# Kernel optimization log

Measured on AMD Instinct MI355X. Metric: run time of the kernel, lower is better.

The kernel has to match this reference:

```python
import jax, jax.numpy as jnp
import numpy as np

N, M, K, C = 1000, 2000, 10, 80
IOU_THRESHOLD = 0.5
EPS = 1e-7


def setup_inputs() -> dict:
    key = jax.random.key(0)
    k1, k2, k3, k4, k5, k6, k7 = jax.random.split(key, 7)
    # pred boxes: realistic xyxy boxes in a 1000x1000 image
    cxy = jax.random.uniform(k1, (N, 2), minval=0.0, maxval=1000.0)
    wh = jax.random.uniform(k2, (N, 2), minval=20.0, maxval=100.0)
    pred_box = jnp.concatenate([cxy - wh / 2, cxy + wh / 2], axis=1)  # [N,4]
    pred = jnp.concatenate([pred_box, jax.random.uniform(k3, (N, 2))], axis=1)  # [N,6]
    # dropout passes: jittered copies of pred boxes (guarantees IoU>0.5 match)
    # followed by M-N random boxes
    copies = pred_box[None, :, :] + jax.random.normal(k4, (K, N, 4)) * 1.0  # [K,N,4]
    rc = jax.random.uniform(k5, (K, M - N, 2), minval=0.0, maxval=1000.0)
    rwh = jax.random.uniform(k6, (K, M - N, 2), minval=20.0, maxval=100.0)
    rand_box = jnp.concatenate([rc - rwh / 2, rc + rwh / 2], axis=2)  # [K,M-N,4]
    boxes = jnp.concatenate([copies, rand_box], axis=1)  # [K,M,4]
    dropout_preds = jnp.concatenate([boxes, jnp.ones((K, M, 2), jnp.float32)], axis=2)
    # per-box class probability rows (softmax-normalized, strictly positive)
    dropout_cls_confs = jax.nn.softmax(jax.random.normal(k7, (K, M, C)), axis=-1)
    return {
        "pred": pred.astype(jnp.float32),
        "dropout_preds": dropout_preds.astype(jnp.float32),
        "dropout_cls_confs": dropout_cls_confs.astype(jnp.float32),
    }


def _pairwise_iou(b1, b2):
    # b1: [N,4] xyxy, b2: [K,M,4] xyxy -> iou [K,N,M]
    ix1 = jnp.maximum(b1[None, :, None, 0], b2[:, None, :, 0])
    iy1 = jnp.maximum(b1[None, :, None, 1], b2[:, None, :, 1])
    ix2 = jnp.minimum(b1[None, :, None, 2], b2[:, None, :, 2])
    iy2 = jnp.minimum(b1[None, :, None, 3], b2[:, None, :, 3])
    inter = jnp.clip(ix2 - ix1, 0.0) * jnp.clip(iy2 - iy1, 0.0)  # [K,N,M]
    area1 = (b1[:, 2] - b1[:, 0]) * (b1[:, 3] - b1[:, 1])  # [N]
    area2 = (b2[..., 2] - b2[..., 0]) * (b2[..., 3] - b2[..., 1])  # [K,M]
    return inter / (area1[None, :, None] + area2[:, None, :] - inter + EPS)


def reference(pred, dropout_preds, dropout_cls_confs):
    n_classes = dropout_cls_confs.shape[-1]
    inv_n = 1.0 / n_classes
    max_entropy = -n_classes * (inv_n * jnp.log(jnp.float32(inv_n)))  # == log(C)

    iou = _pairwise_iou(pred[:, :4], dropout_preds[:, :, :4])  # [K,N,M]
    mask = iou > IOU_THRESHOLD  # [K,N,M]
    matched = jnp.any(mask, axis=-1)  # [K,N] any match in pass k for pred n
    first = jnp.argmax(mask, axis=-1)  # [K,N] index of FIRST match (break semantics)

    # gather the matched class-confidence row per (pass, pred): [K,N,C]
    rows = jnp.take_along_axis(dropout_cls_confs, first[:, :, None], axis=1)
    entropy = -jnp.sum(rows * jnp.log(rows), axis=-1)  # [K,N]
    u = 1.0 - entropy / max_entropy  # [K,N]

    matched_f = matched.astype(u.dtype)
    cnt = jnp.sum(matched_f, axis=0)  # [N]
    sum_u = jnp.sum(u * matched_f, axis=0)  # [N]
    # no-match fallback in original yields NaN (entropy of zeros row)
    semantic_uncertainty = jnp.where(cnt > 0, sum_u / jnp.maximum(cnt, 1.0), jnp.nan)
    return semantic_uncertainty
```

## Files before the change

kernel.cpp:

```cpp
#include <hip/hip_runtime.h>
#include <math.h>

#define N_PRED 1000
#define M_BOX  2000
#define K_PASS 10
#define C_CLS  80
#define IOU_THR 0.5f
#define EPS_IOU 1e-7f

#define P_PRED 4
#define BLK_T  (K_PASS * 64)
#define N_BLK  (N_PRED / P_PRED)

#define IDX_INF 0x7fffffff

__global__ __launch_bounds__(BLK_T)
void ue_cls_kernel(const float* __restrict__ pred,
                   const float* __restrict__ dpreds,
                   const float* __restrict__ dconfs,
                   float* __restrict__ out)
{
    const int k    = threadIdx.x >> 6;
    const int lane = threadIdx.x & 63;
    const int n0   = blockIdx.x * P_PRED;

    __shared__ float s_u[K_PASS][P_PRED];
    __shared__ float s_m[K_PASS][P_PRED];

    float px1[P_PRED], py1[P_PRED], px2[P_PRED], py2[P_PRED], a1[P_PRED];
    #pragma unroll
    for (int p = 0; p < P_PRED; ++p) {
        const float* pr = pred + (n0 + p) * 6;
        px1[p] = pr[0]; py1[p] = pr[1]; px2[p] = pr[2]; py2[p] = pr[3];
        a1[p] = (px2[p] - px1[p]) * (py2[p] - py1[p]);
    }

    const long kbase = (long)k * M_BOX;
    const float2* dp2 = (const float2*)dpreds;

    int firstI[P_PRED];
    #pragma unroll
    for (int p = 0; p < P_PRED; ++p) firstI[p] = IDX_INF;

    const int L = (((n0 + P_PRED - 1) >> 6) << 6) + 64;
    for (int c0 = 0; c0 < L; c0 += 64) {
        const int m = c0 + lane;
        const long i2 = (kbase + m) * 3;
        const float2 a = dp2[i2];
        const float2 b = dp2[i2 + 1];
        const float area2 = (b.x - a.x) * (b.y - a.y);
        #pragma unroll
        for (int p = 0; p < P_PRED; ++p) {
            const float ix1 = fmaxf(px1[p], a.x);
            const float iy1 = fmaxf(py1[p], a.y);
            const float ix2 = fminf(px2[p], b.x);
            const float iy2 = fminf(py2[p], b.y);
            const float inter = fmaxf(ix2 - ix1, 0.0f) * fmaxf(iy2 - iy1, 0.0f);
            const float den = a1[p] + area2 - inter + EPS_IOU;
            if (inter > 0.5f * den) firstI[p] = min(firstI[p], m);
        }
    }
    #pragma unroll
    for (int off = 32; off > 0; off >>= 1) {
        #pragma unroll
        for (int p = 0; p < P_PRED; ++p)
            firstI[p] = min(firstI[p], __shfl_xor(firstI[p], off, 64));
    }

    bool need = false;
    #pragma unroll
    for (int p = 0; p < P_PRED; ++p) need = need || (firstI[p] == IDX_INF);
    if (need) {
        for (int c0 = L; c0 < M_BOX; c0 += 64) {
            const int m = c0 + lane;
            const bool valid = (m < M_BOX);
            const long i2 = (kbase + (valid ? m : M_BOX - 1)) * 3;
            const float2 a = dp2[i2];
            const float2 b = dp2[i2 + 1];
            const float area2 = (b.x - a.x) * (b.y - a.y);
            #pragma unroll
            for (int p = 0; p < P_PRED; ++p) {
                const float ix1 = fmaxf(px1[p], a.x);
                const float iy1 = fmaxf(py1[p], a.y);
                const float ix2 = fminf(px2[p], b.x);
                const float iy2 = fminf(py2[p], b.y);
                const float inter = fmaxf(ix2 - ix1, 0.0f) * fmaxf(iy2 - iy1, 0.0f);
                const float den = a1[p] + area2 - inter + EPS_IOU;
                if (valid && inter > 0.5f * den) firstI[p] = min(firstI[p], m);
            }
        }
        #pragma unroll
        for (int off = 32; off > 0; off >>= 1) {
            #pragma unroll
            for (int p = 0; p < P_PRED; ++p)
                firstI[p] = min(firstI[p], __shfl_xor(firstI[p], off, 64));
        }
    }

    const float inv_n  = 1.0f / (float)C_CLS;
    const float max_en = -(float)C_CLS * (inv_n * logf(inv_n));
    float um[P_PRED], mt[P_PRED];
    #pragma unroll
    for (int p = 0; p < P_PRED; ++p) {
        um[p] = 0.0f; mt[p] = 0.0f;
        if (firstI[p] != IDX_INF) {
            mt[p] = 1.0f;
            const float* row = dconfs + (kbase + firstI[p]) * (long)C_CLS;
            float local = 0.0f;
            {
                const float v = row[lane];
                local -= v * logf(v);
            }
            if (lane < C_CLS - 64) {
                const float v = row[64 + lane];
                local -= v * logf(v);
            }
            #pragma unroll
            for (int off = 32; off > 0; off >>= 1)
                local += __shfl_xor(local, off, 64);
            um[p] = 1.0f - local / max_en;
        }
    }

    if (lane == 0) {
        #pragma unroll
        for (int p = 0; p < P_PRED; ++p) {
            s_u[k][p] = um[p] * mt[p];
            s_m[k][p] = mt[p];
        }
    }
    __syncthreads();

    if (threadIdx.x < P_PRED) {
        const int t = threadIdx.x;
        float cnt = 0.0f, su = 0.0f;
        #pragma unroll
        for (int kk = 0; kk < K_PASS; ++kk) { su += s_u[kk][t]; cnt += s_m[kk][t]; }
        out[n0 + t] = (cnt > 0.0f) ? (su / fmaxf(cnt, 1.0f)) : __builtin_nanf("");
    }
}

extern "C" void kernel_launch(void* const* d_in, const int* in_sizes, int n_in,
                              void* d_out, int out_size, void* d_ws, size_t ws_size,
                              hipStream_t stream) {
    const float* pred   = (const float*)d_in[0];
    const float* dpreds = (const float*)d_in[1];
    const float* dconfs = (const float*)d_in[2];
    float* out = (float*)d_out;

    ue_cls_kernel<<<dim3(N_BLK), dim3(BLK_T), 0, stream>>>(pred, dpreds, dconfs, out);
}
```

Baseline: 70.95 us.

## Process one prediction per block with ballot-based early-exit first-match search

The kernel now launches one block per prediction instead of one block per four predictions, which quadruples the block count and shortens each wave's serial dependency chain. The IoU scan unrolls two 64-column chunks per iteration. It uses a wave ballot with count-trailing-zeros to find the first match and break out immediately, replacing per-lane min tracking followed by a shuffle reduction. The trade-off is that pred-box loads and per-block overhead are repeated four times more often, and imbalance between waves that scan short and long column ranges remains.

```diff
diff --git a/kernel.cpp b/kernel.cpp
--- a/kernel.cpp
+++ b/kernel.cpp
@@ -5,13 +5,9 @@
 #define M_BOX  2000
 #define K_PASS 10
 #define C_CLS  80
-#define IOU_THR 0.5f
 #define EPS_IOU 1e-7f
 
-#define P_PRED 4
 #define BLK_T  (K_PASS * 64)
-#define N_BLK  (N_PRED / P_PRED)
-
 #define IDX_INF 0x7fffffff
 
 __global__ __launch_bounds__(BLK_T)
@@ -20,123 +16,115 @@
                    const float* __restrict__ dconfs,
                    float* __restrict__ out)
 {
+    const int n    = blockIdx.x;
     const int k    = threadIdx.x >> 6;
     const int lane = threadIdx.x & 63;
-    const int n0   = blockIdx.x * P_PRED;
 
-    __shared__ float s_u[K_PASS][P_PRED];
-    __shared__ float s_m[K_PASS][P_PRED];
+    __shared__ float s_u[K_PASS];
+    __shared__ float s_m[K_PASS];
 
-    float px1[P_PRED], py1[P_PRED], px2[P_PRED], py2[P_PRED], a1[P_PRED];
-    #pragma unroll
-    for (int p = 0; p < P_PRED; ++p) {
-        const float* pr = pred + (n0 + p) * 6;
-        px1[p] = pr[0]; py1[p] = pr[1]; px2[p] = pr[2]; py2[p] = pr[3];
-        a1[p] = (px2[p] - px1[p]) * (py2[p] - py1[p]);
+    const float* pr = pred + n * 6;
+    const float px1 = pr[0], py1 = pr[1], px2 = pr[2], py2 = pr[3];
+    const float a1  = (px2 - px1) * (py2 - py1);
+
+    const int kbase = k * M_BOX;
+    const float2* dp2 = (const float2*)dpreds;
+
+    const int L = ((n >> 6) + 1) << 6;
+    int first = IDX_INF;
+    int c0 = 0;
+    for (; c0 < L; c0 += 128) {
+        const int iA = (kbase + c0 + lane) * 3;
+        const int iB = iA + 64 * 3;
+        const float2 aA = dp2[iA];
+        const float2 bA = dp2[iA + 1];
+        const float2 aB = dp2[iB];
+        const float2 bB = dp2[iB + 1];
+
+        const float areaA = (bA.x - aA.x) * (bA.y - aA.y);
+        const float ix1A = fmaxf(px1, aA.x);
+        const float iy1A = fmaxf(py1, aA.y);
+        const float ix2A = fminf(px2, bA.x);
+        const float iy2A = fminf(py2, bA.y);
+        const float interA = fmaxf(ix2A - ix1A, 0.0f) * fmaxf(iy2A - iy1A, 0.0f);
+        const float denA = a1 + areaA - interA + EPS_IOU;
+
+        const float areaB = (bB.x - aB.x) * (bB.y - aB.y);
+        const float ix1B = fmaxf(px1, aB.x);
+        const float iy1B = fmaxf(py1, aB.y);
+        const float ix2B = fminf(px2, bB.x);
+        const float iy2B = fminf(py2, bB.y);
+        const float interB = fmaxf(ix2B - ix1B, 0.0f) * fmaxf(iy2B - iy1B, 0.0f);
+        const float denB = a1 + areaB - interB + EPS_IOU;
+
+        const unsigned long long hitA = __ballot(interA > 0.5f * denA);
+        const unsigned long long hitB = __ballot(interB > 0.5f * denB);
+        if (hitA) { first = c0 + __builtin_ctzll(hitA); break; }
+        if (hitB) { first = c0 + 64 + __builtin_ctzll(hitB); break; }
     }
 
-    const long kbase = (long)k * M_BOX;
-    const float2* dp2 = (const float2*)dpreds;
+    if (first == IDX_INF) {
+        for (; c0 < M_BOX; c0 += 128) {
+            const int mA = c0 + lane;
+            const int mB = mA + 64;
+            const bool vA = (mA < M_BOX);
+            const bool vB = (mB < M_BOX);
+            const int iA = (kbase + (vA ? mA : 0)) * 3;
+            const int iB = (kbase + (vB ? mB : 0)) * 3;
+            const float2 aA = dp2[iA];
+            const float2 bA = dp2[iA + 1];
+            const float2 aB = dp2[iB];
+            const float2 bB = dp2[iB + 1];
 
-    int firstI[P_PRED];
-    #pragma unroll
-    for (int p = 0; p < P_PRED; ++p) firstI[p] = IDX_INF;
+            const float areaA = (bA.x - aA.x) * (bA.y - aA.y);
+            const float interA = fmaxf(fminf(px2, bA.x) - fmaxf(px1, aA.x), 0.0f)
+                               * fmaxf(fminf(py2, bA.y) - fmaxf(py1, aA.y), 0.0f);
+            const float denA = a1 + areaA - interA + EPS_IOU;
 
-    const int L = (((n0 + P_PRED - 1) >> 6) << 6) + 64;
-    for (int c0 = 0; c0 < L; c0 += 64) {
-        const int m = c0 + lane;
-        const long i2 = (kbase + m) * 3;
-        const float2 a = dp2[i2];
-        const float2 b = dp2[i2 + 1];
-        const float area2 = (b.x - a.x) * (b.y - a.y);
-        #pragma unroll
-        for (int p = 0; p < P_PRED; ++p) {
-            const float ix1 = fmaxf(px1[p], a.x);
-            const float iy1 = fmaxf(py1[p], a.y);
-            const float ix2 = fminf(px2[p], b.x);
-            const float iy2 = fminf(py2[p], b.y);
-            const float inter = fmaxf(ix2 - ix1, 0.0f) * fmaxf(iy2 - iy1, 0.0f);
-            const float den = a1[p] + area2 - inter + EPS_IOU;
-            if (inter > 0.5f * den) firstI[p] = min(firstI[p], m);
-        }
-    }
-    #pragma unroll
-    for (int off = 32; off > 0; off >>= 1) {
-        #pragma unroll
-        for (int p = 0; p < P_PRED; ++p)
-            firstI[p] = min(firstI[p], __shfl_xor(firstI[p], off, 64));
-    }
+            const float areaB = (bB.x - aB.x) * (bB.y - aB.y);
+            const float interB = fmaxf(fminf(px2, bB.x) - fmaxf(px1, aB.x), 0.0f)
+                               * fmaxf(fminf(py2, bB.y) - fmaxf(py1, aB.y), 0.0f);
+            const float denB = a1 + areaB - interB + EPS_IOU;
 
-    bool need = false;
-    #pragma unroll
-    for (int p = 0; p < P_PRED; ++p) need = need || (firstI[p] == IDX_INF);
-    if (need) {
-        for (int c0 = L; c0 < M_BOX; c0 += 64) {
-            const int m = c0 + lane;
-            const bool valid = (m < M_BOX);
-            const long i2 = (kbase + (valid ? m : M_BOX - 1)) * 3;
-            const float2 a = dp2[i2];
-            const float2 b = dp2[i2 + 1];
-            const float area2 = (b.x - a.x) * (b.y - a.y);
-            #pragma unroll
-            for (int p = 0; p < P_PRED; ++p) {
-                const float ix1 = fmaxf(px1[p], a.x);
-                const float iy1 = fmaxf(py1[p], a.y);
-                const float ix2 = fminf(px2[p], b.x);
-                const float iy2 = fminf(py2[p], b.y);
-                const float inter = fmaxf(ix2 - ix1, 0.0f) * fmaxf(iy2 - iy1, 0.0f);
-                const float den = a1[p] + area2 - inter + EPS_IOU;
-                if (valid && inter > 0.5f * den) firstI[p] = min(firstI[p], m);
-            }
-        }
-        #pragma unroll
-        for (int off = 32; off > 0; off >>= 1) {
-            #pragma unroll
-            for (int p = 0; p < P_PRED; ++p)
-                firstI[p] = min(firstI[p], __shfl_xor(firstI[p], off, 64));
+            const unsigned long long hitA = __ballot(vA && (interA > 0.5f * denA));
+            const unsigned long long hitB = __ballot(vB && (interB > 0.5f * denB));
+            if (hitA) { first = c0 + __builtin_ctzll(hitA); break; }
+            if (hitB) { first = c0 + 64 + __builtin_ctzll(hitB); break; }
         }
     }
 
     const float inv_n  = 1.0f / (float)C_CLS;
     const float max_en = -(float)C_CLS * (inv_n * logf(inv_n));
-    float um[P_PRED], mt[P_PRED];
-    #pragma unroll
-    for (int p = 0; p < P_PRED; ++p) {
-        um[p] = 0.0f; mt[p] = 0.0f;
-        if (firstI[p] != IDX_INF) {
-            mt[p] = 1.0f;
-            const float* row = dconfs + (kbase + firstI[p]) * (long)C_CLS;
-            float local = 0.0f;
-            {
-                const float v = row[lane];
-                local -= v * logf(v);
-            }
-            if (lane < C_CLS - 64) {
-                const float v = row[64 + lane];
-                local -= v * logf(v);
-            }
-            #pragma unroll
-            for (int off = 32; off > 0; off >>= 1)
-                local += __shfl_xor(local, off, 64);
-            um[p] = 1.0f - local / max_en;
+    float u = 0.0f, mt = 0.0f;
+    if (first != IDX_INF) {
+        mt = 1.0f;
+        const float* row = dconfs + (kbase + first) * (long)C_CLS;
+        float local = 0.0f;
+        {
+            const float v = row[lane];
+            local -= v * logf(v);
         }
+        if (lane < C_CLS - 64) {
+            const float v = row[64 + lane];
+            local -= v * logf(v);
+        }
+        #pragma unroll
+        for (int off = 32; off > 0; off >>= 1)
+            local += __shfl_xor(local, off, 64);
+        u = 1.0f - local / max_en;
     }
 
     if (lane == 0) {
-        #pragma unroll
-        for (int p = 0; p < P_PRED; ++p) {
-            s_u[k][p] = um[p] * mt[p];
-            s_m[k][p] = mt[p];
-        }
+        s_u[k] = u * mt;
+        s_m[k] = mt;
     }
     __syncthreads();
 
-    if (threadIdx.x < P_PRED) {
-        const int t = threadIdx.x;
+    if (threadIdx.x == 0) {
         float cnt = 0.0f, su = 0.0f;
         #pragma unroll
-        for (int kk = 0; kk < K_PASS; ++kk) { su += s_u[kk][t]; cnt += s_m[kk][t]; }
-        out[n0 + t] = (cnt > 0.0f) ? (su / fmaxf(cnt, 1.0f)) : __builtin_nanf("");
+        for (int kk = 0; kk < K_PASS; ++kk) { su += s_u[kk]; cnt += s_m[kk]; }
+        out[n] = (cnt > 0.0f) ? (su / fmaxf(cnt, 1.0f)) : __builtin_nanf("");
     }
 }
 
@@ -148,5 +136,5 @@
     const float* dconfs = (const float*)d_in[2];
     float* out = (float*)d_out;
 
-    ue_cls_kernel<<<dim3(N_BLK), dim3(BLK_T), 0, stream>>>(pred, dpreds, dconfs, out);
+    ue_cls_kernel<<<dim3(N_PRED), dim3(BLK_T), 0, stream>>>(pred, dpreds, dconfs, out);
 }
```

Result: faster. 69.26 us (-2.4%).

## Split IoU scan across waves per pass with 16-pred tiles and separate reduce kernel

Applied to the files above, without the earlier changes.

Restructures the work decomposition: each block now handles one dropout pass and a tile of 16 predictions, with four waves splitting the box chunks and combining first-match indices through shared memory. Per-pass results go to a workspace, and a second small kernel averages over passes. This gives more reuse of each loaded box across predictions and spreads the serial chunk loop over waves. The cost is an extra kernel launch, workspace traffic, extra barriers and higher register pressure from 16-wide per-thread arrays.

```diff
diff --git a/kernel.cpp b/kernel.cpp
--- a/kernel.cpp
+++ b/kernel.cpp
@@ -5,139 +5,168 @@
 #define M_BOX  2000
 #define K_PASS 10
 #define C_CLS  80
-#define IOU_THR 0.5f
 #define EPS_IOU 1e-7f
 
-#define P_PRED 4
-#define BLK_T  (K_PASS * 64)
-#define N_BLK  (N_PRED / P_PRED)
-
+#define T_PRED 16
+#define NT ((N_PRED + T_PRED - 1) / T_PRED)
+#define WAVES 4
+#define BLK (WAVES * 64)
+#define MCHUNKS ((M_BOX + 63) >> 6)
 #define IDX_INF 0x7fffffff
 
-__global__ __launch_bounds__(BLK_T)
-void ue_cls_kernel(const float* __restrict__ pred,
-                   const float* __restrict__ dpreds,
-                   const float* __restrict__ dconfs,
-                   float* __restrict__ out)
+__global__ __launch_bounds__(BLK)
+void ue_scan_kernel(const float* __restrict__ pred,
+                    const float* __restrict__ dpreds,
+                    const float* __restrict__ dconfs,
+                    float* __restrict__ ws_u,
+                    float* __restrict__ ws_mt)
 {
-    const int k    = threadIdx.x >> 6;
+    const int tile = blockIdx.x;
+    const int k    = blockIdx.y;
+    const int w    = threadIdx.x >> 6;
     const int lane = threadIdx.x & 63;
-    const int n0   = blockIdx.x * P_PRED;
+    const int base = tile * T_PRED;
 
-    __shared__ float s_u[K_PASS][P_PRED];
-    __shared__ float s_m[K_PASS][P_PRED];
+    __shared__ int s_min[WAVES][T_PRED];
 
-    float px1[P_PRED], py1[P_PRED], px2[P_PRED], py2[P_PRED], a1[P_PRED];
+    float px1[T_PRED], py1[T_PRED], px2[T_PRED], py2[T_PRED], a1[T_PRED];
     #pragma unroll
-    for (int p = 0; p < P_PRED; ++p) {
-        const float* pr = pred + (n0 + p) * 6;
+    for (int p = 0; p < T_PRED; ++p) {
+        int np = base + p; if (np > N_PRED - 1) np = N_PRED - 1;
+        const float* pr = pred + np * 6;
         px1[p] = pr[0]; py1[p] = pr[1]; px2[p] = pr[2]; py2[p] = pr[3];
         a1[p] = (px2[p] - px1[p]) * (py2[p] - py1[p]);
     }
 
-    const long kbase = (long)k * M_BOX;
+    const int kbase = k * M_BOX;
     const float2* dp2 = (const float2*)dpreds;
 
-    int firstI[P_PRED];
+    const int maxn = (base + T_PRED - 1 < N_PRED - 1) ? base + T_PRED - 1 : N_PRED - 1;
+    const int nchunks = (maxn >> 6) + 1;
+
+    int mi[T_PRED];
     #pragma unroll
-    for (int p = 0; p < P_PRED; ++p) firstI[p] = IDX_INF;
+    for (int p = 0; p < T_PRED; ++p) mi[p] = IDX_INF;
 
-    const int L = (((n0 + P_PRED - 1) >> 6) << 6) + 64;
-    for (int c0 = 0; c0 < L; c0 += 64) {
-        const int m = c0 + lane;
-        const long i2 = (kbase + m) * 3;
+    for (int c = w; c < nchunks; c += WAVES) {
+        const int m = (c << 6) + lane;
+        const int i2 = (kbase + m) * 3;
         const float2 a = dp2[i2];
         const float2 b = dp2[i2 + 1];
         const float area2 = (b.x - a.x) * (b.y - a.y);
         #pragma unroll
-        for (int p = 0; p < P_PRED; ++p) {
+        for (int p = 0; p < T_PRED; ++p) {
             const float ix1 = fmaxf(px1[p], a.x);
             const float iy1 = fmaxf(py1[p], a.y);
             const float ix2 = fminf(px2[p], b.x);
             const float iy2 = fminf(py2[p], b.y);
             const float inter = fmaxf(ix2 - ix1, 0.0f) * fmaxf(iy2 - iy1, 0.0f);
             const float den = a1[p] + area2 - inter + EPS_IOU;
-            if (inter > 0.5f * den) firstI[p] = min(firstI[p], m);
+            if ((base + p < N_PRED) && (inter > 0.5f * den)) mi[p] = min(mi[p], m);
         }
     }
+
     #pragma unroll
     for (int off = 32; off > 0; off >>= 1) {
         #pragma unroll
-        for (int p = 0; p < P_PRED; ++p)
-            firstI[p] = min(firstI[p], __shfl_xor(firstI[p], off, 64));
+        for (int p = 0; p < T_PRED; ++p)
+            mi[p] = min(mi[p], __shfl_xor(mi[p], off, 64));
     }
+    if (lane == 0) {
+        #pragma unroll
+        for (int p = 0; p < T_PRED; ++p) s_min[w][p] = mi[p];
+    }
+    __syncthreads();
 
     bool need = false;
     #pragma unroll
-    for (int p = 0; p < P_PRED; ++p) need = need || (firstI[p] == IDX_INF);
+    for (int p = 0; p < T_PRED; ++p) {
+        int v = min(min(s_min[0][p], s_min[1][p]), min(s_min[2][p], s_min[3][p]));
+        need = need || ((base + p < N_PRED) && v == IDX_INF);
+    }
     if (need) {
-        for (int c0 = L; c0 < M_BOX; c0 += 64) {
-            const int m = c0 + lane;
+        for (int c = nchunks + w; c < MCHUNKS; c += WAVES) {
+            const int m = (c << 6) + lane;
             const bool valid = (m < M_BOX);
-            const long i2 = (kbase + (valid ? m : M_BOX - 1)) * 3;
+            const int i2 = (kbase + (valid ? m : M_BOX - 1)) * 3;
             const float2 a = dp2[i2];
             const float2 b = dp2[i2 + 1];
             const float area2 = (b.x - a.x) * (b.y - a.y);
             #pragma unroll
-            for (int p = 0; p < P_PRED; ++p) {
+            for (int p = 0; p < T_PRED; ++p) {
                 const float ix1 = fmaxf(px1[p], a.x);
                 const float iy1 = fmaxf(py1[p], a.y);
                 const float ix2 = fminf(px2[p], b.x);
                 const float iy2 = fminf(py2[p], b.y);
                 const float inter = fmaxf(ix2 - ix1, 0.0f) * fmaxf(iy2 - iy1, 0.0f);
                 const float den = a1[p] + area2 - inter + EPS_IOU;
-                if (valid && inter > 0.5f * den) firstI[p] = min(firstI[p], m);
+                if (valid && (base + p < N_PRED) && (inter > 0.5f * den))
+                    mi[p] = min(mi[p], m);
             }
         }
         #pragma unroll
         for (int off = 32; off > 0; off >>= 1) {
             #pragma unroll
-            for (int p = 0; p < P_PRED; ++p)
-                firstI[p] = min(firstI[p], __shfl_xor(firstI[p], off, 64));
+            for (int p = 0; p < T_PRED; ++p)
+                mi[p] = min(mi[p], __shfl_xor(mi[p], off, 64));
         }
+        __syncthreads();
+        if (lane == 0) {
+            #pragma unroll
+            for (int p = 0; p < T_PRED; ++p) s_min[w][p] = mi[p];
+        }
+        __syncthreads();
     }
 
     const float inv_n  = 1.0f / (float)C_CLS;
     const float max_en = -(float)C_CLS * (inv_n * logf(inv_n));
-    float um[P_PRED], mt[P_PRED];
     #pragma unroll
-    for (int p = 0; p < P_PRED; ++p) {
-        um[p] = 0.0f; mt[p] = 0.0f;
-        if (firstI[p] != IDX_INF) {
-            mt[p] = 1.0f;
-            const float* row = dconfs + (kbase + firstI[p]) * (long)C_CLS;
-            float local = 0.0f;
-            {
-                const float v = row[lane];
-                local -= v * logf(v);
+    for (int j = 0; j < T_PRED / WAVES; ++j) {
+        const int p = w + j * WAVES;
+        const int n = base + p;
+        if (n < N_PRED) {
+            const int f = min(min(s_min[0][p], s_min[1][p]),
+                              min(s_min[2][p], s_min[3][p]));
+            float u = 0.0f, mt = 0.0f;
+            if (f != IDX_INF) {
+                mt = 1.0f;
+                const float* row = dconfs + (size_t)(kbase + f) * C_CLS;
+                float local = 0.0f;
+                {
+                    const float v = row[lane];
+                    local -= v * logf(v);
+                }
+                if (lane < C_CLS - 64) {
+                    const float v = row[64 + lane];
+                    local -= v * logf(v);
+                }
+                #pragma unroll
+                for (int off = 32; off > 0; off >>= 1)
+                    local += __shfl_xor(local, off, 64);
+                u = 1.0f - local / max_en;
             }
-            if (lane < C_CLS - 64) {
-                const float v = row[64 + lane];
-                local -= v * logf(v);
+            if (lane == 0) {
+                ws_u[k * N_PRED + n]  = u * mt;
+                ws_mt[k * N_PRED + n] = mt;
             }
-            #pragma unroll
-            for (int off = 32; off > 0; off >>= 1)
-                local += __shfl_xor(local, off, 64);
-            um[p] = 1.0f - local / max_en;
         }
     }
+}
 
-    if (lane == 0) {
-        #pragma unroll
-        for (int p = 0; p < P_PRED; ++p) {
-            s_u[k][p] = um[p] * mt[p];
-            s_m[k][p] = mt[p];
-        }
+__global__ __launch_bounds__(256)
+void ue_final_kernel(const float* __restrict__ ws_u,
+                     const float* __restrict__ ws_mt,
+                     float* __restrict__ out)
+{
+    const int n = blockIdx.x * 256 + threadIdx.x;
+    if (n >= N_PRED) return;
+    float su = 0.0f, cnt = 0.0f;
+    #pragma unroll
+    for (int kk = 0; kk < K_PASS; ++kk) {
+        su  += ws_u[kk * N_PRED + n];
+        cnt += ws_mt[kk * N_PRED + n];
     }
-    __syncthreads();
-
-    if (threadIdx.x < P_PRED) {
-        const int t = threadIdx.x;
-        float cnt = 0.0f, su = 0.0f;
-        #pragma unroll
-        for (int kk = 0; kk < K_PASS; ++kk) { su += s_u[kk][t]; cnt += s_m[kk][t]; }
-        out[n0 + t] = (cnt > 0.0f) ? (su / fmaxf(cnt, 1.0f)) : __builtin_nanf("");
-    }
+    out[n] = (cnt > 0.0f) ? (su / fmaxf(cnt, 1.0f)) : __builtin_nanf("");
 }
 
 extern "C" void kernel_launch(void* const* d_in, const int* in_sizes, int n_in,
@@ -146,7 +175,13 @@
     const float* pred   = (const float*)d_in[0];
     const float* dpreds = (const float*)d_in[1];
     const float* dconfs = (const float*)d_in[2];
-    float* out = (float*)d_out;
+    float* out  = (float*)d_out;
+    float* ws   = (float*)d_ws;
+    float* ws_u  = ws;
+    float* ws_mt = ws + K_PASS * N_PRED;
 
-    ue_cls_kernel<<<dim3(N_BLK), dim3(BLK_T), 0, stream>>>(pred, dpreds, dconfs, out);
+    ue_scan_kernel<<<dim3(NT, K_PASS), dim3(BLK), 0, stream>>>(
+        pred, dpreds, dconfs, ws_u, ws_mt);
+    ue_final_kernel<<<dim3((N_PRED + 255) / 256), dim3(256), 0, stream>>>(
+        ws_u, ws_mt, out);
 }
```

New measurement: 77.39 us. +9.1%, slower.

## Prefetch diagonal class rows, halve preds per block, reverse block order

Applied to the files above, without the earlier changes.

Each block now handles two predictions instead of four, which doubles the block count and shortens the prefix scan each block performs. Block order is reversed so the blocks with the longest scans (high n0) are scheduled first. Each wavefront speculatively loads the class-confidence row at index n, since the test data tends to match there, so the dependent gather after the IoU search is skipped when the first match equals n. 64-bit index arithmetic is narrowed to 32-bit. The trade-off is extra loads that are wasted when the guess misses, plus redundant per-block setup.

```diff
diff --git a/kernel.cpp b/kernel.cpp
--- a/kernel.cpp
+++ b/kernel.cpp
@@ -5,10 +5,9 @@
 #define M_BOX  2000
 #define K_PASS 10
 #define C_CLS  80
-#define IOU_THR 0.5f
 #define EPS_IOU 1e-7f
 
-#define P_PRED 4
+#define P_PRED 2
 #define BLK_T  (K_PASS * 64)
 #define N_BLK  (N_PRED / P_PRED)
 
@@ -22,7 +21,7 @@
 {
     const int k    = threadIdx.x >> 6;
     const int lane = threadIdx.x & 63;
-    const int n0   = blockIdx.x * P_PRED;
+    const int n0   = (N_BLK - 1 - blockIdx.x) * P_PRED;
 
     __shared__ float s_u[K_PASS][P_PRED];
     __shared__ float s_m[K_PASS][P_PRED];
@@ -35,8 +34,16 @@
         a1[p] = (px2[p] - px1[p]) * (py2[p] - py1[p]);
     }
 
-    const long kbase = (long)k * M_BOX;
+    const int kbase = k * M_BOX;
     const float2* dp2 = (const float2*)dpreds;
+
+    float sv0[P_PRED], sv1[P_PRED];
+    #pragma unroll
+    for (int p = 0; p < P_PRED; ++p) {
+        const float* row = dconfs + (size_t)(kbase + n0 + p) * C_CLS;
+        sv0[p] = row[lane];
+        sv1[p] = (lane < C_CLS - 64) ? row[64 + lane] : 0.0f;
+    }
 
     int firstI[P_PRED];
     #pragma unroll
@@ -45,7 +52,7 @@
     const int L = (((n0 + P_PRED - 1) >> 6) << 6) + 64;
     for (int c0 = 0; c0 < L; c0 += 64) {
         const int m = c0 + lane;
-        const long i2 = (kbase + m) * 3;
+        const int i2 = (kbase + m) * 3;
         const float2 a = dp2[i2];
         const float2 b = dp2[i2 + 1];
         const float area2 = (b.x - a.x) * (b.y - a.y);
@@ -74,7 +81,7 @@
         for (int c0 = L; c0 < M_BOX; c0 += 64) {
             const int m = c0 + lane;
             const bool valid = (m < M_BOX);
-            const long i2 = (kbase + (valid ? m : M_BOX - 1)) * 3;
+            const int i2 = (kbase + (valid ? m : M_BOX - 1)) * 3;
             const float2 a = dp2[i2];
             const float2 b = dp2[i2 + 1];
             const float area2 = (b.x - a.x) * (b.y - a.y);
@@ -105,16 +112,16 @@
         um[p] = 0.0f; mt[p] = 0.0f;
         if (firstI[p] != IDX_INF) {
             mt[p] = 1.0f;
-            const float* row = dconfs + (kbase + firstI[p]) * (long)C_CLS;
-            float local = 0.0f;
-            {
-                const float v = row[lane];
-                local -= v * logf(v);
+            float v0, v1 = 0.0f;
+            if (firstI[p] == n0 + p) {
+                v0 = sv0[p]; v1 = sv1[p];
+            } else {
+                const float* row = dconfs + (size_t)(kbase + firstI[p]) * C_CLS;
+                v0 = row[lane];
+                if (lane < C_CLS - 64) v1 = row[64 + lane];
             }
-            if (lane < C_CLS - 64) {
-                const float v = row[64 + lane];
-                local -= v * logf(v);
-            }
+            float local = -v0 * logf(v0);
+            if (lane < C_CLS - 64) local -= v1 * logf(v1);
             #pragma unroll
             for (int off = 32; off > 0; off >>= 1)
                 local += __shfl_xor(local, off, 64);
```

Measured after the change: 67.51 us. 1.05x faster.
